# Kernel optimization log

Hardware: AMD Instinct MI355X
Metric: run time of the kernel (lower is better)

## Reference

```python
import jax, jax.numpy as jnp
import numpy as np

B, T, C, H = 8, 2048, 1024, 128  # batch, seq, n_embed, head_size

def setup_inputs() -> dict:
    key = jax.random.key(0)
    ks = jax.random.split(key, 6)
    s = 1.0 / np.sqrt(C)
    return {
        "x": jax.random.normal(ks[0], (B, T, C), dtype=jnp.float32),
        "Wk": jax.random.uniform(ks[1], (C, H), minval=-s, maxval=s, dtype=jnp.float32),
        "Wq": jax.random.uniform(ks[2], (C, H), minval=-s, maxval=s, dtype=jnp.float32),
        "Wv": jax.random.uniform(ks[3], (C, H), minval=-s, maxval=s, dtype=jnp.float32),
        "Wp": jax.random.uniform(ks[4], (H, H), minval=-1/np.sqrt(H), maxval=1/np.sqrt(H), dtype=jnp.float32),
        "bp": jax.random.uniform(ks[5], (H,), minval=-1/np.sqrt(H), maxval=1/np.sqrt(H), dtype=jnp.float32),
    }

def reference(x, Wk, Wq, Wv, Wp, bp):
    # x: [B,T,C]; projections are bias-free
    k = x @ Wk  # [B,T,H]
    q = x @ Wq
    v = x @ Wv
    scale = jnp.asarray(H, x.dtype) ** -0.5
    scores = jnp.einsum('bqh,bkh->bqk', q, k) * scale  # [B,T,T]
    causal = jnp.tril(jnp.ones((T, T), dtype=bool))
    scores = jnp.where(causal, scores, jnp.finfo(x.dtype).min)
    w = jax.nn.softmax(scores, axis=-1)
    out = jnp.einsum('bqk,bkh->bqh', w, v)  # [B,T,H]
    return out @ Wp + bp
```

## Files before the change

kernel.cpp:

```cpp
#include <hip/hip_runtime.h>

constexpr int Bz = 8, Tt = 2048, Cc = 1024, Hh = 128;
constexpr int Mrows = Bz * Tt;
constexpr float kScale = 0.08838834764831843f;

typedef float f32x4 __attribute__((ext_vector_type(4)));
typedef short s16x8 __attribute__((ext_vector_type(8)));
typedef short s16x4 __attribute__((ext_vector_type(4)));
typedef unsigned short u16;

static __device__ __forceinline__ u16 f2bf(float f) {
    union { float f; unsigned int u; } c; c.f = f;
    unsigned int u = c.u;
    unsigned int r = (u + 0x7fffu + ((u >> 16) & 1u)) >> 16;
    return (u16)r;
}
static __device__ __forceinline__ float bf2f(u16 x) {
    union { unsigned int u; float f; } c; c.u = ((unsigned int)x) << 16;
    return c.f;
}

__global__ __launch_bounds__(256) void convw_kernel(
    const float* __restrict__ Wq, const float* __restrict__ Wk,
    const float* __restrict__ Wv, const float* __restrict__ Wp,
    u16* __restrict__ wt, u16* __restrict__ wpt)
{
    int i = blockIdx.x * 256 + threadIdx.x;
    if (i < 393216) {
        int z = i >> 17, r = i & 131071;
        int n = r >> 10, k = r & 1023;
        const float* W = (z == 0) ? Wq : (z == 1) ? Wk : Wv;
        wt[i] = f2bf(W[k * Hh + n]);
    } else {
        int r2 = i - 393216;
        int n = r2 >> 7, k = r2 & 127;
        wpt[r2] = f2bf(Wp[k * Hh + n]);
    }
}

__global__ __launch_bounds__(256, 2)
void qkv_fused(
    const float* __restrict__ x, const u16* __restrict__ wt,
    u16* __restrict__ qo, u16* __restrict__ ko, u16* __restrict__ vt)
{
    __shared__ __align__(16) u16 as[64 * 64];

    const int tid  = threadIdx.x;
    const int m0   = blockIdx.x * 64;
    const int lane = tid & 63, wid = tid >> 6;
    const int l15  = lane & 15, l4 = lane >> 4;
    const int bb   = m0 >> 11;
    const int t0   = m0 & 2047;

    f32x4 acc[4][6];
#pragma unroll
    for (int mi = 0; mi < 4; ++mi)
#pragma unroll
        for (int ni = 0; ni < 6; ++ni) {
            f32x4 z4 = {0.f, 0.f, 0.f, 0.f};
            acc[mi][ni] = z4;
        }

    for (int k0 = 0; k0 < Cc; k0 += 64) {
#pragma unroll
        for (int u = 0; u < 4; ++u) {
            int idx = tid + u * 256;
            int m = idx >> 4, kf4 = (idx & 15) * 4;
            float4 xv = *reinterpret_cast<const float4*>(
                &x[(size_t)(m0 + m) * Cc + k0 + kf4]);
            s16x4 bv;
            bv[0] = (short)f2bf(xv.x); bv[1] = (short)f2bf(xv.y);
            bv[2] = (short)f2bf(xv.z); bv[3] = (short)f2bf(xv.w);
            *reinterpret_cast<s16x4*>(&as[m * 64 + (kf4 ^ ((m & 7) << 3))]) = bv;
        }
        s16x8 bfr[6][2];
#pragma unroll
        for (int ni = 0; ni < 6; ++ni) {
            int c = wid * 96 + ni * 16;
            int z = c >> 7, nloc = (c & 127) + l15;
            const u16* wb = wt + (size_t)z * 131072 + (size_t)nloc * 1024 + k0;
#pragma unroll
            for (int ks = 0; ks < 2; ++ks)
                bfr[ni][ks] = *reinterpret_cast<const s16x8*>(&wb[ks * 32 + l4 * 8]);
        }
        __syncthreads();

        s16x8 af[4][2];
#pragma unroll
        for (int mi = 0; mi < 4; ++mi) {
            int r = mi * 16 + l15;
#pragma unroll
            for (int ks = 0; ks < 2; ++ks)
                af[mi][ks] = *reinterpret_cast<const s16x8*>(
                    &as[r * 64 + ((ks * 32 + l4 * 8) ^ ((r & 7) << 3))]);
        }
#pragma unroll
        for (int mi = 0; mi < 4; ++mi)
#pragma unroll
            for (int ni = 0; ni < 6; ++ni)
#pragma unroll
                for (int ks = 0; ks < 2; ++ks)
                    acc[mi][ni] = __builtin_amdgcn_mfma_f32_16x16x32_bf16(
                        af[mi][ks], bfr[ni][ks], acc[mi][ni], 0, 0, 0);
        __syncthreads();
    }

#pragma unroll
    for (int mi = 0; mi < 4; ++mi)
#pragma unroll
        for (int ni = 0; ni < 6; ++ni) {
            int c = wid * 96 + ni * 16;
            int z = c >> 7, colz = (c & 127) + l15;
            if (z < 2) {
                u16* outp = (z == 0) ? qo : ko;
#pragma unroll
                for (int r = 0; r < 4; ++r) {
                    int row = m0 + mi * 16 + l4 * 4 + r;
                    outp[(size_t)row * Hh + colz] = f2bf(acc[mi][ni][r]);
                }
            } else {
                int trow = t0 + mi * 16 + l4 * 4;
                s16x4 pk;
#pragma unroll
                for (int r = 0; r < 4; ++r) pk[r] = (short)f2bf(acc[mi][ni][r]);
                *reinterpret_cast<s16x4*>(
                    &vt[((size_t)bb * Hh + colz) * Tt + trow]) = pk;
            }
        }
}

__global__ __launch_bounds__(256, 4)
void attn_kernel(
    const u16* __restrict__ q, const u16* __restrict__ k,
    const u16* __restrict__ vt,
    u16* __restrict__ Opart, float* __restrict__ Mp, float* __restrict__ Lp)
{
    __shared__ __align__(16) char arena[37888];
    u16* ksl = reinterpret_cast<u16*>(arena);
    u16* vsl = reinterpret_cast<u16*>(arena + 16384);
    u16* psl = reinterpret_cast<u16*>(arena + 32768);
    float* Om  = reinterpret_cast<float*>(arena);
    float* ml2 = reinterpret_cast<float*>(arena + 33792);

    const int tid = threadIdx.x, lane = tid & 63, wid = tid >> 6;
    const int l15 = lane & 15, l4 = lane >> 4;
    const int wq = wid >> 1, half = wid & 1;
    const int bid = blockIdx.x;
    const int b = bid & 7;
    const int rest = bid >> 3;
    const int qt = 63 - (rest >> 1);
    const int split = rest & 1;
    const int q0 = qt * 32;
    const int ntf = (qt + 2) >> 1;
    const int lo = (ntf * split) >> 1;
    const int hi = (ntf * (split + 1)) >> 1;

    const u16* qb = q  + (size_t)b * Tt * Hh;
    const u16* kb = k  + (size_t)b * Tt * Hh;
    const u16* vb = vt + (size_t)b * Hh * Tt;

    const int qrow = q0 + wq * 16 + l15;
    s16x8 qf[4];
#pragma unroll
    for (int ks = 0; ks < 4; ++ks)
        qf[ks] = *reinterpret_cast<const s16x8*>(
            &qb[(size_t)qrow * Hh + ks * 32 + l4 * 8]);

    f32x4 o[8];
#pragma unroll
    for (int nh = 0; nh < 8; ++nh) { f32x4 z4 = {0.f,0.f,0.f,0.f}; o[nh] = z4; }
    float mreg = -1e30f, lreg = 0.f;

    const int kr_s  = tid >> 2, kc_s = (tid & 3) * 4;
    const int vh_s  = tid >> 1, vc_s = (tid & 1) * 4;
    u16* ps = psl + wid * 640;

    for (int j = lo; j < hi; ++j) {
        const int kv0 = j * 64;

#pragma unroll
        for (int i = 0; i < 4; ++i) {
            s16x8 tk = *reinterpret_cast<const s16x8*>(
                &kb[(size_t)(kv0 + kr_s) * Hh + (kc_s + i) * 8]);
            *reinterpret_cast<s16x8*>(
                &ksl[kr_s * 128 + (((kc_s + i) * 8) ^ ((kr_s & 7) << 3))]) = tk;
        }
#pragma unroll
        for (int i = 0; i < 4; ++i) {
            s16x8 tv = *reinterpret_cast<const s16x8*>(
                &vb[(size_t)vh_s * Tt + kv0 + (vc_s + i) * 8]);
            *reinterpret_cast<s16x8*>(
                &vsl[vh_s * 64 + (((vc_s + i) * 8) ^ ((vh_s & 7) << 3))]) = tv;
        }
        __syncthreads();

        f32x4 sacc[2];
#pragma unroll
        for (int nf = 0; nf < 2; ++nf) { f32x4 z4 = {0.f,0.f,0.f,0.f}; sacc[nf] = z4; }
#pragma unroll
        for (int nf = 0; nf < 2; ++nf) {
            const int kr = half * 32 + nf * 16 + l15;
#pragma unroll
            for (int ks = 0; ks < 4; ++ks) {
                s16x8 kfrag = *reinterpret_cast<const s16x8*>(
                    &ksl[kr * 128 + ((ks * 32 + l4 * 8) ^ ((kr & 7) << 3))]);
                sacc[nf] = __builtin_amdgcn_mfma_f32_16x16x32_bf16(
                    kfrag, qf[ks], sacc[nf], 0, 0, 0);
            }
        }

        const bool diag = (j == ntf - 1);
        float pv2[2][4];
#pragma unroll
        for (int nf = 0; nf < 2; ++nf)
#pragma unroll
            for (int r = 0; r < 4; ++r) {
                float s = sacc[nf][r] * kScale;
                if (diag) {
                    int kvg = kv0 + half * 32 + nf * 16 + l4 * 4 + r;
                    if (kvg > qrow) s = -1e30f;
                }
                pv2[nf][r] = s;
            }
        float mx = fmaxf(fmaxf(fmaxf(pv2[0][0], pv2[0][1]), fmaxf(pv2[0][2], pv2[0][3])),
                         fmaxf(fmaxf(pv2[1][0], pv2[1][1]), fmaxf(pv2[1][2], pv2[1][3])));
        mx = fmaxf(mx, __shfl_xor(mx, 16));
        mx = fmaxf(mx, __shfl_xor(mx, 32));
        const float mold = mreg;
        const float mnew = fmaxf(mold, mx);
        const float scl = __expf(mold - mnew);
        mreg = mnew;
        float rs = 0.f;
#pragma unroll
        for (int nf = 0; nf < 2; ++nf)
#pragma unroll
            for (int r = 0; r < 4; ++r) {
                float pp = __expf(pv2[nf][r] - mnew);
                pv2[nf][r] = pp; rs += pp;
            }
        rs += __shfl_xor(rs, 16);
        rs += __shfl_xor(rs, 32);
        lreg = lreg * scl + rs;

        if (!__all(mold == mnew)) {
            float sclr[4];
#pragma unroll
            for (int r = 0; r < 4; ++r) sclr[r] = __shfl(scl, l4 * 4 + r);
#pragma unroll
            for (int nh = 0; nh < 8; ++nh)
#pragma unroll
                for (int r = 0; r < 4; ++r) o[nh][r] *= sclr[r];
        }

#pragma unroll
        for (int nf = 0; nf < 2; ++nf) {
            s16x4 pk4;
#pragma unroll
            for (int r = 0; r < 4; ++r) pk4[r] = (short)f2bf(pv2[nf][r]);
            *reinterpret_cast<s16x4*>(&ps[l15 * 40 + nf * 16 + l4 * 4]) = pk4;
        }
        s16x8 pa = *reinterpret_cast<const s16x8*>(&ps[l15 * 40 + l4 * 8]);

#pragma unroll
        for (int nh = 0; nh < 8; ++nh) {
            const int hr = nh * 16 + l15;
            s16x8 vfrag = *reinterpret_cast<const s16x8*>(
                &vsl[hr * 64 + ((half * 32 + l4 * 8) ^ ((hr & 7) << 3))]);
            o[nh] = __builtin_amdgcn_mfma_f32_16x16x32_bf16(
                pa, vfrag, o[nh], 0, 0, 0);
        }
        __syncthreads();
    }

#pragma unroll
    for (int nh = 0; nh < 8; ++nh)
#pragma unroll
        for (int r = 0; r < 4; ++r)
            Om[((wid * 16) + l4 * 4 + r) * 132 + nh * 16 + l15] = o[nh][r];
    if (lane < 16) {
        ml2[wid * 32 + lane] = mreg;
        ml2[wid * 32 + 16 + lane] = lreg;
    }
    __syncthreads();

    {
        const int row = tid >> 3, ch = tid & 7;
        const int rg = row >> 4, r16 = row & 15;
        const int w0 = rg * 2, w1 = rg * 2 + 1;
        float m0v = ml2[w0 * 32 + r16], m1v = ml2[w1 * 32 + r16];
        float M = fmaxf(m0v, m1v);
        float f0 = __expf(m0v - M), f1 = __expf(m1v - M);
        float L = f0 * ml2[w0 * 32 + 16 + r16] + f1 * ml2[w1 * 32 + 16 + r16];
        const size_t gm = (size_t)b * Tt + q0 + row;
        union { u16 u[8]; s16x8 v; } pk0, pk1;
#pragma unroll
        for (int c = 0; c < 8; ++c) {
            float a = f0 * Om[(w0 * 16 + r16) * 132 + ch * 16 + c]
                    + f1 * Om[(w1 * 16 + r16) * 132 + ch * 16 + c];
            pk0.u[c] = f2bf(a);
        }
#pragma unroll
        for (int c = 0; c < 8; ++c) {
            float a = f0 * Om[(w0 * 16 + r16) * 132 + ch * 16 + 8 + c]
                    + f1 * Om[(w1 * 16 + r16) * 132 + ch * 16 + 8 + c];
            pk1.u[c] = f2bf(a);
        }
        u16* op = Opart + ((size_t)split * Mrows + gm) * 128 + ch * 16;
        *reinterpret_cast<s16x8*>(op) = pk0.v;
        *reinterpret_cast<s16x8*>(op + 8) = pk1.v;
        if (ch == 0) {
            Mp[split * Mrows + gm] = M;
            Lp[split * Mrows + gm] = L;
        }
    }
}

__global__ __launch_bounds__(256) void merge_proj(
    const u16* __restrict__ Opart, const float* __restrict__ Mp,
    const float* __restrict__ Lp, const u16* __restrict__ wpt,
    const float* __restrict__ bp, float* __restrict__ O)
{
    __shared__ __align__(16) u16 pm[64 * 136];
    __shared__ float f0s[64], f1s[64], invs[64];

    const int tid = threadIdx.x, lane = tid & 63, wid = tid >> 6;
    const int l15 = lane & 15, l4 = lane >> 4;
    const int m0r = blockIdx.x * 64;

    if (tid < 64) {
        float m0v = Mp[m0r + tid], m1v = Mp[Mrows + m0r + tid];
        float M = fmaxf(m0v, m1v);
        float a0 = __expf(m0v - M), a1 = __expf(m1v - M);
        float L = a0 * Lp[m0r + tid] + a1 * Lp[Mrows + m0r + tid];
        f0s[tid] = a0; f1s[tid] = a1; invs[tid] = 1.f / L;
    }
    __syncthreads();

#pragma unroll
    for (int u = 0; u < 4; ++u) {
        int idx = tid + u * 256;
        int row = idx >> 4, g = idx & 15;
        const size_t base = (size_t)(m0r + row) * 128 + g * 8;
        s16x8 p0 = *reinterpret_cast<const s16x8*>(&Opart[base]);
        s16x8 p1 = *reinterpret_cast<const s16x8*>(
            &Opart[(size_t)Mrows * 128 + base]);
        float a0 = f0s[row], a1 = f1s[row], inv = invs[row];
        union { u16 u[8]; s16x8 v; } pk;
#pragma unroll
        for (int c = 0; c < 8; ++c) {
            float v0 = bf2f((u16)p0[c]), v1 = bf2f((u16)p1[c]);
            pk.u[c] = f2bf((a0 * v0 + a1 * v1) * inv);
        }
        *reinterpret_cast<s16x8*>(&pm[row * 136 + g * 8]) = pk.v;
    }
    __syncthreads();

    {
        const int row2 = wid * 16 + l15;
        s16x8 af2[4];
#pragma unroll
        for (int ks = 0; ks < 4; ++ks)
            af2[ks] = *reinterpret_cast<const s16x8*>(
                &pm[row2 * 136 + ks * 32 + l4 * 8]);
#pragma unroll
        for (int ng = 0; ng < 8; ++ng) {
            const int ncol = ng * 16 + l15;
            f32x4 pacc = {0.f, 0.f, 0.f, 0.f};
#pragma unroll
            for (int ks = 0; ks < 4; ++ks) {
                s16x8 wf = *reinterpret_cast<const s16x8*>(
                    &wpt[(size_t)ncol * 128 + ks * 32 + l4 * 8]);
                pacc = __builtin_amdgcn_mfma_f32_16x16x32_bf16(
                    af2[ks], wf, pacc, 0, 0, 0);
            }
            float bias = bp[ncol];
#pragma unroll
            for (int r = 0; r < 4; ++r)
                O[(size_t)(m0r + wid * 16 + l4 * 4 + r) * Hh + ncol] =
                    pacc[r] + bias;
        }
    }
}

extern "C" void kernel_launch(void* const* d_in, const int* in_sizes, int n_in,
                              void* d_out, int out_size, void* d_ws, size_t ws_size,
                              hipStream_t stream) {
    const float* x  = (const float*)d_in[0];
    const float* Wk = (const float*)d_in[1];
    const float* Wq = (const float*)d_in[2];
    const float* Wv = (const float*)d_in[3];
    const float* Wp = (const float*)d_in[4];
    const float* bp = (const float*)d_in[5];
    float* out = (float*)d_out;

    u16* wtb = (u16*)d_ws;
    u16* wpt = wtb + 393216;
    u16* qw  = wpt + 16384;
    u16* kw  = qw + (size_t)Mrows * Hh;
    u16* vtb = kw + (size_t)Mrows * Hh;
    u16* opart = vtb + (size_t)Mrows * Hh;
    float* Mpart = (float*)(opart + (size_t)2 * Mrows * Hh);
    float* Lpart = Mpart + 2 * Mrows;

    convw_kernel<<<1600, 256, 0, stream>>>(Wq, Wk, Wv, Wp, wtb, wpt);
    qkv_fused<<<Mrows / 64, 256, 0, stream>>>(x, wtb, qw, kw, vtb);
    attn_kernel<<<1024, 256, 0, stream>>>(qw, kw, vtb, opart, Mpart, Lpart);
    merge_proj<<<Mrows / 64, 256, 0, stream>>>(opart, Mpart, Lpart, wpt, bp, out);
}
```

Measured before the change: 85.91 us.

## Double-buffer x tile in QKV projection with smaller row tiles and deeper K

Rewrites the QKV projection main loop to use two shared-memory buffers. The next x chunk is loaded into registers and converted to bf16 while the MFMAs for the current chunk run, which removes one barrier per iteration and hides global load latency. The row tile shrinks from 64 to 32 and the K step grows from 64 to 128, doubling the grid to 512 blocks. The trade-off is that each block now reads the full weight slice for only 32 rows, so total weight traffic from L2 doubles.

After: 100.7 us. 17.2% more time.

```diff
diff --git a/kernel.cpp b/kernel.cpp
--- a/kernel.cpp
+++ b/kernel.cpp
@@ -43,70 +43,101 @@
     const float* __restrict__ x, const u16* __restrict__ wt,
     u16* __restrict__ qo, u16* __restrict__ ko, u16* __restrict__ vt)
 {
-    __shared__ __align__(16) u16 as[64 * 64];
+    __shared__ __align__(16) u16 as[2][32 * 128];
 
     const int tid  = threadIdx.x;
-    const int m0   = blockIdx.x * 64;
+    const int m0   = blockIdx.x * 32;
     const int lane = tid & 63, wid = tid >> 6;
     const int l15  = lane & 15, l4 = lane >> 4;
     const int bb   = m0 >> 11;
     const int t0   = m0 & 2047;
 
-    f32x4 acc[4][6];
-#pragma unroll
-    for (int mi = 0; mi < 4; ++mi)
+    const int m_s  = tid >> 3;
+    const int c4_s = (tid & 7) * 4;
+
+    f32x4 acc[2][6];
+#pragma unroll
+    for (int mi = 0; mi < 2; ++mi)
 #pragma unroll
         for (int ni = 0; ni < 6; ++ni) {
             f32x4 z4 = {0.f, 0.f, 0.f, 0.f};
             acc[mi][ni] = z4;
         }
 
-    for (int k0 = 0; k0 < Cc; k0 += 64) {
-#pragma unroll
-        for (int u = 0; u < 4; ++u) {
-            int idx = tid + u * 256;
-            int m = idx >> 4, kf4 = (idx & 15) * 4;
-            float4 xv = *reinterpret_cast<const float4*>(
-                &x[(size_t)(m0 + m) * Cc + k0 + kf4]);
-            s16x4 bv;
-            bv[0] = (short)f2bf(xv.x); bv[1] = (short)f2bf(xv.y);
-            bv[2] = (short)f2bf(xv.z); bv[3] = (short)f2bf(xv.w);
-            *reinterpret_cast<s16x4*>(&as[m * 64 + (kf4 ^ ((m & 7) << 3))]) = bv;
-        }
-        s16x8 bfr[6][2];
+#pragma unroll
+    for (int u = 0; u < 4; ++u) {
+        int kf4 = (c4_s + u * 32) * 4 % 128;
+        int kcol = (tid & 7) * 4 + u * 32;
+        float4 xv = *reinterpret_cast<const float4*>(
+            &x[(size_t)(m0 + m_s) * Cc + kcol * 1]);
+        s16x4 bv;
+        bv[0] = (short)f2bf(xv.x); bv[1] = (short)f2bf(xv.y);
+        bv[2] = (short)f2bf(xv.z); bv[3] = (short)f2bf(xv.w);
+        *reinterpret_cast<s16x4*>(
+            &as[0][m_s * 128 + (kcol ^ ((m_s & 7) << 3))]) = bv;
+        (void)kf4;
+    }
+
+    for (int j = 0; j < 8; ++j) {
+        const int buf = j & 1;
+        const int k0 = j * 128;
+        __syncthreads();
+
+        s16x8 af[2][4];
+#pragma unroll
+        for (int mi = 0; mi < 2; ++mi) {
+            int r = mi * 16 + l15;
+#pragma unroll
+            for (int ks = 0; ks < 4; ++ks)
+                af[mi][ks] = *reinterpret_cast<const s16x8*>(
+                    &as[buf][r * 128 + ((ks * 32 + l4 * 8) ^ ((r & 7) << 3))]);
+        }
+
+        float4 a_next[4];
+        if (j < 7) {
+#pragma unroll
+            for (int u = 0; u < 4; ++u) {
+                int kcol = (tid & 7) * 4 + u * 32;
+                a_next[u] = *reinterpret_cast<const float4*>(
+                    &x[(size_t)(m0 + m_s) * Cc + k0 + 128 + kcol]);
+            }
+        }
+
+        s16x8 bfr[6][4];
 #pragma unroll
         for (int ni = 0; ni < 6; ++ni) {
             int c = wid * 96 + ni * 16;
             int z = c >> 7, nloc = (c & 127) + l15;
             const u16* wb = wt + (size_t)z * 131072 + (size_t)nloc * 1024 + k0;
 #pragma unroll
-            for (int ks = 0; ks < 2; ++ks)
+            for (int ks = 0; ks < 4; ++ks)
                 bfr[ni][ks] = *reinterpret_cast<const s16x8*>(&wb[ks * 32 + l4 * 8]);
         }
-        __syncthreads();
-
-        s16x8 af[4][2];
-#pragma unroll
-        for (int mi = 0; mi < 4; ++mi) {
-            int r = mi * 16 + l15;
-#pragma unroll
-            for (int ks = 0; ks < 2; ++ks)
-                af[mi][ks] = *reinterpret_cast<const s16x8*>(
-                    &as[r * 64 + ((ks * 32 + l4 * 8) ^ ((r & 7) << 3))]);
-        }
-#pragma unroll
-        for (int mi = 0; mi < 4; ++mi)
+
+#pragma unroll
+        for (int mi = 0; mi < 2; ++mi)
 #pragma unroll
             for (int ni = 0; ni < 6; ++ni)
 #pragma unroll
-                for (int ks = 0; ks < 2; ++ks)
+                for (int ks = 0; ks < 4; ++ks)
                     acc[mi][ni] = __builtin_amdgcn_mfma_f32_16x16x32_bf16(
                         af[mi][ks], bfr[ni][ks], acc[mi][ni], 0, 0, 0);
-        __syncthreads();
-    }
-
-#pragma unroll
-    for (int mi = 0; mi < 4; ++mi)
+
+        if (j < 7) {
+#pragma unroll
+            for (int u = 0; u < 4; ++u) {
+                int kcol = (tid & 7) * 4 + u * 32;
+                s16x4 bv;
+                bv[0] = (short)f2bf(a_next[u].x); bv[1] = (short)f2bf(a_next[u].y);
+                bv[2] = (short)f2bf(a_next[u].z); bv[3] = (short)f2bf(a_next[u].w);
+                *reinterpret_cast<s16x4*>(
+                    &as[buf ^ 1][m_s * 128 + (kcol ^ ((m_s & 7) << 3))]) = bv;
+            }
+        }
+    }
+
+#pragma unroll
+    for (int mi = 0; mi < 2; ++mi)
 #pragma unroll
         for (int ni = 0; ni < 6; ++ni) {
             int c = wid * 96 + ni * 16;
@@ -403,7 +434,7 @@
     float* Lpart = Mpart + 2 * Mrows;
 
     convw_kernel<<<1600, 256, 0, stream>>>(Wq, Wk, Wv, Wp, wtb, wpt);
-    qkv_fused<<<Mrows / 64, 256, 0, stream>>>(x, wtb, qw, kw, vtb);
+    qkv_fused<<<Mrows / 32, 256, 0, stream>>>(x, wtb, qw, kw, vtb);
     attn_kernel<<<1024, 256, 0, stream>>>(qw, kw, vtb, opart, Mpart, Lpart);
     merge_proj<<<Mrows / 64, 256, 0, stream>>>(opart, Mpart, Lpart, wpt, bp, out);
 }
```
